# Kernel tuning notes

Hardware: AMD Instinct MI355X
Metric: run time of the kernel (lower is better)

Reference implementation:

```python
import jax, jax.numpy as jnp
import numpy as np

Q, S, D = 8192, 30, 512
THRESH = 30


def setup_inputs() -> dict:
    key = jax.random.key(0)
    ks = jax.random.split(key, 8)
    return {
        "query_encode": jax.random.normal(ks[0], (Q, D), jnp.float32),
        "support_encode": jax.random.normal(ks[1], (S, D), jnp.float32),
        # binary CTR-style labels in {0,1}
        "support_y": jnp.round(jax.random.uniform(ks[2], (1, S), jnp.float32)),
        "support_predict": jax.random.normal(ks[3], (S,), jnp.float32),
        "query_predict": jax.random.normal(ks[4], (Q,), jnp.float32),
        "fc1_w": jax.random.normal(ks[5], (D,), jnp.float32) / np.sqrt(D),
        "fc1_b": jnp.zeros((), jnp.float32),
        # AdjustLayer params: scale init 6, bias init 0, shape [THRESH, 1]
        "adjust_scale": jnp.full((THRESH, 1), 6.0, jnp.float32),
        "adjust_bias": jnp.zeros((THRESH, 1), jnp.float32),
        "num_samples": S,
    }


def reference(query_encode, support_encode, support_y, support_predict,
              query_predict, fc1_w, fc1_b, adjust_scale, adjust_bias,
              num_samples):
    # Pairwise L1 distance: [Q, S, D]
    distance = jnp.abs(query_encode[:, None, :] - support_encode[None, :, :])
    # Linear scorer over feature dim -> [Q, S]
    similar_score = jnp.einsum("qsd,d->qs", distance, fc1_w) + fc1_b
    attn = jax.nn.softmax(similar_score, axis=1)  # softmax over support dim
    # Residual of support labels vs predictor output: [1, S]
    delta_y = support_y - jax.nn.sigmoid(support_predict)[None, :]
    delta_y_hat = jnp.sum(delta_y * attn, axis=1)  # [Q]
    # AdjustLayer: indexed scale/bias (index is a static int here)
    scale = jnp.abs(adjust_scale[num_samples - 1, 0])
    bias = adjust_bias[num_samples - 1, 0]
    prediction = delta_y_hat * scale + bias + query_predict  # [Q]
    # Mean L2 distance to support set: [Q]
    mean_l2 = jnp.mean(jnp.sqrt(jnp.sum(distance ** 2, axis=-1)), axis=-1)
    return prediction, mean_l2
```

## Files before the change

kernel.cpp:

```cpp
#include <hip/hip_runtime.h>
#include <math.h>


#define QN 8192
#define SN 30
#define DN 512
#define BLK 512
#define QT 16
#define SCHUNK 10
#define NPASS 3
#define SROW 580
#define PRW 17
#define PSTR 31

__global__ __launch_bounds__(BLK, 2)
void resus_one(const float* __restrict__ query,
               const float* __restrict__ support,
               const float* __restrict__ support_y,
               const float* __restrict__ support_pr,
               const float* __restrict__ query_pr,
               const float* __restrict__ fc1_w,
               const float* __restrict__ adj_scale,
               const float* __restrict__ adj_bias,
               const int*   __restrict__ num_samples,
               float* __restrict__ out)
{
    __shared__ float  sp[SCHUNK * SROW];
    __shared__ float  praw_sc[SCHUNK * QT * PRW];
    __shared__ float  praw_sq[SCHUNK * QT * PRW];
    __shared__ float2 part[QT * PSTR];

    const int tid   = threadIdx.x;
    const int ql    = tid & 15;
    const int dseg  = (tid >> 4) & 15;
    const int shalf = tid >> 8;
    const int q     = blockIdx.x * QT + ql;

    const float* qp = query + (size_t)q * DN + dseg * 32;
    float4 q0 = *reinterpret_cast<const float4*>(qp +  0);
    float4 q1 = *reinterpret_cast<const float4*>(qp +  4);
    float4 q2 = *reinterpret_cast<const float4*>(qp +  8);
    float4 q3 = *reinterpret_cast<const float4*>(qp + 12);
    float4 q4 = *reinterpret_cast<const float4*>(qp + 16);
    float4 q5 = *reinterpret_cast<const float4*>(qp + 20);
    float4 q6 = *reinterpret_cast<const float4*>(qp + 24);
    float4 q7 = *reinterpret_cast<const float4*>(qp + 28);
    const float* wp = fc1_w + dseg * 32;
    float4 w0 = *reinterpret_cast<const float4*>(wp +  0);
    float4 w1 = *reinterpret_cast<const float4*>(wp +  4);
    float4 w2 = *reinterpret_cast<const float4*>(wp +  8);
    float4 w3 = *reinterpret_cast<const float4*>(wp + 12);
    float4 w4 = *reinterpret_cast<const float4*>(wp + 16);
    float4 w5 = *reinterpret_cast<const float4*>(wp + 20);
    float4 w6 = *reinterpret_cast<const float4*>(wp + 24);
    float4 w7 = *reinterpret_cast<const float4*>(wp + 28);

#define PIN4(V) asm volatile("" : "+v"((V).x), "+v"((V).y), "+v"((V).z), "+v"((V).w))
    PIN4(q0); PIN4(q1); PIN4(q2); PIN4(q3);
    PIN4(q4); PIN4(q5); PIN4(q6); PIN4(q7);
    PIN4(w0); PIN4(w1); PIN4(w2); PIN4(w3);
    PIN4(w4); PIN4(w5); PIN4(w6); PIN4(w7);
#undef PIN4

#define ACC4(QV, WV, SV) { float d_; \
    d_ = (QV).x - (SV).x; sc = fmaf((WV).x, fabsf(d_), sc); sq = fmaf(d_, d_, sq); \
    d_ = (QV).y - (SV).y; sc = fmaf((WV).y, fabsf(d_), sc); sq = fmaf(d_, d_, sq); \
    d_ = (QV).z - (SV).z; sc = fmaf((WV).z, fabsf(d_), sc); sq = fmaf(d_, d_, sq); \
    d_ = (QV).w - (SV).w; sc = fmaf((WV).w, fabsf(d_), sc); sq = fmaf(d_, d_, sq); }

    const int sbase = dseg * 36;
    const int pbase = ql * PRW + dseg;
    const int sl0   = shalf * (SCHUNK / 2);

    for (int pass = 0; pass < NPASS; ++pass) {
        __syncthreads();

        const float4* sg = reinterpret_cast<const float4*>(
            support + (size_t)pass * SCHUNK * DN);
        for (int i = tid; i < SCHUNK * 128; i += BLK) {
            const int row = i >> 7, c4 = i & 127;
            *reinterpret_cast<float4*>(
                sp + row * SROW + 36 * (c4 >> 3) + 4 * (c4 & 7)) = sg[i];
        }
        __syncthreads();

#pragma unroll
        for (int k = 0; k < SCHUNK / 2; ++k) {
            const int sl = sl0 + k;
            const float* sr = sp + sl * SROW + sbase;
            const float4 s0 = *reinterpret_cast<const float4*>(sr +  0);
            const float4 s1 = *reinterpret_cast<const float4*>(sr +  4);
            const float4 s2 = *reinterpret_cast<const float4*>(sr +  8);
            const float4 s3 = *reinterpret_cast<const float4*>(sr + 12);
            const float4 s4 = *reinterpret_cast<const float4*>(sr + 16);
            const float4 s5 = *reinterpret_cast<const float4*>(sr + 20);
            const float4 s6 = *reinterpret_cast<const float4*>(sr + 24);
            const float4 s7 = *reinterpret_cast<const float4*>(sr + 28);

            float sc = 0.0f, sq = 0.0f;
            ACC4(q0, w0, s0) ACC4(q1, w1, s1)
            ACC4(q2, w2, s2) ACC4(q3, w3, s3)
            ACC4(q4, w4, s4) ACC4(q5, w5, s5)
            ACC4(q6, w6, s6) ACC4(q7, w7, s7)

            praw_sc[sl * (QT * PRW) + pbase] = sc;
            praw_sq[sl * (QT * PRW) + pbase] = sq;
        }
        __syncthreads();

        if (tid < SCHUNK * QT) {
            const int sl = tid >> 4, qq = tid & 15;
            const int b = sl * (QT * PRW) + qq * PRW;
            float sc = 0.0f, sq = 0.0f;
#pragma unroll
            for (int d = 0; d < 16; ++d) {
                sc += praw_sc[b + d];
                sq += praw_sq[b + d];
            }
            part[qq * PSTR + pass * SCHUNK + sl] = make_float2(sc, sq);
        }
    }
#undef ACC4
    __syncthreads();

    const int grp  = tid >> 5;
    const int s32  = tid & 31;
    const bool valid = (s32 < SN);
    const int  si  = valid ? s32 : 0;

    float dy = 0.0f;
    if (valid)
        dy = support_y[s32] - 1.0f / (1.0f + expf(-support_pr[s32]));

    const int ns = num_samples[0];
    const float ascale = fabsf(adj_scale[ns - 1]);
    const float abias  = adj_bias[ns - 1];

    const int qg = blockIdx.x * QT + grp;
    const float2 pr = part[grp * PSTR + si];

    float scv = valid ? pr.x : -1e30f;
    float ssv = valid ? pr.y : 0.0f;

    float m = scv;
#pragma unroll
    for (int off = 16; off >= 1; off >>= 1)
        m = fmaxf(m, __shfl_xor(m, off));

    float e   = valid ? expf(scv - m) : 0.0f;
    float den = e;
    float num = dy * e;
    float l2  = valid ? sqrtf(ssv) : 0.0f;
#pragma unroll
    for (int off = 16; off >= 1; off >>= 1) {
        den += __shfl_xor(den, off);
        num += __shfl_xor(num, off);
        l2  += __shfl_xor(l2,  off);
    }

    if (s32 == 0) {
        out[qg]      = num / den * ascale + abias + query_pr[qg];
        out[QN + qg] = l2 * (1.0f / (float)SN);
    }
}

extern "C" void kernel_launch(void* const* d_in, const int* in_sizes, int n_in,
                              void* d_out, int out_size, void* d_ws, size_t ws_size,
                              hipStream_t stream)
{
    const float* query      = (const float*)d_in[0];
    const float* support    = (const float*)d_in[1];
    const float* support_y  = (const float*)d_in[2];
    const float* support_pr = (const float*)d_in[3];
    const float* query_pr   = (const float*)d_in[4];
    const float* fc1_w      = (const float*)d_in[5];
    const float* adj_scale  = (const float*)d_in[7];
    const float* adj_bias   = (const float*)d_in[8];
    const int*   num_s      = (const int*)d_in[9];
    float* out = (float*)d_out;

    dim3 grid(QN / QT);
    hipLaunchKernelGGL(resus_one, grid, dim3(BLK), 0, stream,
                       query, support, support_y, support_pr, query_pr,
                       fc1_w, adj_scale, adj_bias, num_s, out);
}
```

Measured before the change: 95.10 us.

## Compute two queries per thread to reuse support LDS loads, smaller support chunks

Each thread now handles two queries over a 16-wide feature segment instead of one query over 32, so each support vector loaded from shared memory is reused for two query rows, halving LDS reads per FMA. The support chunk shrinks to 6 rows over 5 passes with a new padded layout. The partial-sum layout changes accordingly, and the per-pass reduction now sums 32 segments instead of 16. The tradeoffs are more passes and barriers and a longer serial reduction per pass.

```diff
diff --git a/kernel.cpp b/kernel.cpp
--- a/kernel.cpp
+++ b/kernel.cpp
@@ -7,10 +7,11 @@
 #define DN 512
 #define BLK 512
 #define QT 16
-#define SCHUNK 10
-#define NPASS 3
-#define SROW 580
-#define PRW 17
+#define SCHUNK 6
+#define NPASS 5
+#define SROW 644
+#define PQS 17
+#define SLSTR 545
 #define PSTR 31
 
 __global__ __launch_bounds__(BLK, 2)
@@ -26,50 +27,46 @@
                float* __restrict__ out)
 {
     __shared__ float  sp[SCHUNK * SROW];
-    __shared__ float  praw_sc[SCHUNK * QT * PRW];
-    __shared__ float  praw_sq[SCHUNK * QT * PRW];
+    __shared__ float  praw_sc[SCHUNK * SLSTR];
+    __shared__ float  praw_sq[SCHUNK * SLSTR];
     __shared__ float2 part[QT * PSTR];
 
     const int tid   = threadIdx.x;
-    const int ql    = tid & 15;
-    const int dseg  = (tid >> 4) & 15;
+    const int qpair = tid & 7;
+    const int dseg  = (tid >> 3) & 31;
     const int shalf = tid >> 8;
-    const int q     = blockIdx.x * QT + ql;
+    const int qA    = blockIdx.x * QT + qpair;
+    const int qB    = qA + 8;
 
-    const float* qp = query + (size_t)q * DN + dseg * 32;
-    float4 q0 = *reinterpret_cast<const float4*>(qp +  0);
-    float4 q1 = *reinterpret_cast<const float4*>(qp +  4);
-    float4 q2 = *reinterpret_cast<const float4*>(qp +  8);
-    float4 q3 = *reinterpret_cast<const float4*>(qp + 12);
-    float4 q4 = *reinterpret_cast<const float4*>(qp + 16);
-    float4 q5 = *reinterpret_cast<const float4*>(qp + 20);
-    float4 q6 = *reinterpret_cast<const float4*>(qp + 24);
-    float4 q7 = *reinterpret_cast<const float4*>(qp + 28);
-    const float* wp = fc1_w + dseg * 32;
+    const float* qpA = query + (size_t)qA * DN + dseg * 16;
+    float4 a0 = *reinterpret_cast<const float4*>(qpA +  0);
+    float4 a1 = *reinterpret_cast<const float4*>(qpA +  4);
+    float4 a2 = *reinterpret_cast<const float4*>(qpA +  8);
+    float4 a3 = *reinterpret_cast<const float4*>(qpA + 12);
+    const float* qpB = query + (size_t)qB * DN + dseg * 16;
+    float4 b0 = *reinterpret_cast<const float4*>(qpB +  0);
+    float4 b1 = *reinterpret_cast<const float4*>(qpB +  4);
+    float4 b2 = *reinterpret_cast<const float4*>(qpB +  8);
+    float4 b3 = *reinterpret_cast<const float4*>(qpB + 12);
+    const float* wp = fc1_w + dseg * 16;
     float4 w0 = *reinterpret_cast<const float4*>(wp +  0);
     float4 w1 = *reinterpret_cast<const float4*>(wp +  4);
     float4 w2 = *reinterpret_cast<const float4*>(wp +  8);
     float4 w3 = *reinterpret_cast<const float4*>(wp + 12);
-    float4 w4 = *reinterpret_cast<const float4*>(wp + 16);
-    float4 w5 = *reinterpret_cast<const float4*>(wp + 20);
-    float4 w6 = *reinterpret_cast<const float4*>(wp + 24);
-    float4 w7 = *reinterpret_cast<const float4*>(wp + 28);
 
 #define PIN4(V) asm volatile("" : "+v"((V).x), "+v"((V).y), "+v"((V).z), "+v"((V).w))
-    PIN4(q0); PIN4(q1); PIN4(q2); PIN4(q3);
-    PIN4(q4); PIN4(q5); PIN4(q6); PIN4(q7);
+    PIN4(a0); PIN4(a1); PIN4(a2); PIN4(a3);
+    PIN4(b0); PIN4(b1); PIN4(b2); PIN4(b3);
     PIN4(w0); PIN4(w1); PIN4(w2); PIN4(w3);
-    PIN4(w4); PIN4(w5); PIN4(w6); PIN4(w7);
 #undef PIN4
 
-#define ACC4(QV, WV, SV) { float d_; \
-    d_ = (QV).x - (SV).x; sc = fmaf((WV).x, fabsf(d_), sc); sq = fmaf(d_, d_, sq); \
-    d_ = (QV).y - (SV).y; sc = fmaf((WV).y, fabsf(d_), sc); sq = fmaf(d_, d_, sq); \
-    d_ = (QV).z - (SV).z; sc = fmaf((WV).z, fabsf(d_), sc); sq = fmaf(d_, d_, sq); \
-    d_ = (QV).w - (SV).w; sc = fmaf((WV).w, fabsf(d_), sc); sq = fmaf(d_, d_, sq); }
+#define ACC4(QV, WV, SV, SC, SQ) { float d_; \
+    d_ = (QV).x - (SV).x; SC = fmaf((WV).x, fabsf(d_), SC); SQ = fmaf(d_, d_, SQ); \
+    d_ = (QV).y - (SV).y; SC = fmaf((WV).y, fabsf(d_), SC); SQ = fmaf(d_, d_, SQ); \
+    d_ = (QV).z - (SV).z; SC = fmaf((WV).z, fabsf(d_), SC); SQ = fmaf(d_, d_, SQ); \
+    d_ = (QV).w - (SV).w; SC = fmaf((WV).w, fabsf(d_), SC); SQ = fmaf(d_, d_, SQ); }
 
-    const int sbase = dseg * 36;
-    const int pbase = ql * PRW + dseg;
+    const int sbase = dseg * 20;
     const int sl0   = shalf * (SCHUNK / 2);
 
     for (int pass = 0; pass < NPASS; ++pass) {
@@ -80,7 +77,7 @@
         for (int i = tid; i < SCHUNK * 128; i += BLK) {
             const int row = i >> 7, c4 = i & 127;
             *reinterpret_cast<float4*>(
-                sp + row * SROW + 36 * (c4 >> 3) + 4 * (c4 & 7)) = sg[i];
+                sp + row * SROW + 20 * (c4 >> 2) + 4 * (c4 & 3)) = sg[i];
         }
         __syncthreads();
 
@@ -92,30 +89,29 @@
             const float4 s1 = *reinterpret_cast<const float4*>(sr +  4);
             const float4 s2 = *reinterpret_cast<const float4*>(sr +  8);
             const float4 s3 = *reinterpret_cast<const float4*>(sr + 12);
-            const float4 s4 = *reinterpret_cast<const float4*>(sr + 16);
-            const float4 s5 = *reinterpret_cast<const float4*>(sr + 20);
-            const float4 s6 = *reinterpret_cast<const float4*>(sr + 24);
-            const float4 s7 = *reinterpret_cast<const float4*>(sr + 28);
 
-            float sc = 0.0f, sq = 0.0f;
-            ACC4(q0, w0, s0) ACC4(q1, w1, s1)
-            ACC4(q2, w2, s2) ACC4(q3, w3, s3)
-            ACC4(q4, w4, s4) ACC4(q5, w5, s5)
-            ACC4(q6, w6, s6) ACC4(q7, w7, s7)
+            float scA = 0.0f, sqA = 0.0f, scB = 0.0f, sqB = 0.0f;
+            ACC4(a0, w0, s0, scA, sqA) ACC4(a1, w1, s1, scA, sqA)
+            ACC4(a2, w2, s2, scA, sqA) ACC4(a3, w3, s3, scA, sqA)
+            ACC4(b0, w0, s0, scB, sqB) ACC4(b1, w1, s1, scB, sqB)
+            ACC4(b2, w2, s2, scB, sqB) ACC4(b3, w3, s3, scB, sqB)
 
-            praw_sc[sl * (QT * PRW) + pbase] = sc;
-            praw_sq[sl * (QT * PRW) + pbase] = sq;
+            const int pb = sl * SLSTR + dseg * PQS + qpair;
+            praw_sc[pb]     = scA;
+            praw_sq[pb]     = sqA;
+            praw_sc[pb + 8] = scB;
+            praw_sq[pb + 8] = sqB;
         }
         __syncthreads();
 
         if (tid < SCHUNK * QT) {
             const int sl = tid >> 4, qq = tid & 15;
-            const int b = sl * (QT * PRW) + qq * PRW;
+            const int b = sl * SLSTR + qq;
             float sc = 0.0f, sq = 0.0f;
 #pragma unroll
-            for (int d = 0; d < 16; ++d) {
-                sc += praw_sc[b + d];
-                sq += praw_sq[b + d];
+            for (int d = 0; d < 32; ++d) {
+                sc += praw_sc[b + d * PQS];
+                sq += praw_sq[b + d * PQS];
             }
             part[qq * PSTR + pass * SCHUNK + sl] = make_float2(sc, sq);
         }
```

Result: no change. 95.66 us (+0.6%).
